# Performance work log

Hardware: AMD Instinct MI355X
Metric: run time of the kernel (lower is better)

## Reference

```python
import jax, jax.numpy as jnp
import numpy as np

BATCH = 16384
IN = 1024
OUT = 1024
SIGMA_MIN = 0.1
SIGMA_MAX = 1.0


def setup_inputs() -> dict:
    key = jax.random.key(0)
    k0, k1, k2, k3 = jax.random.split(key, 4)
    x = jax.random.normal(k0, (BATCH, IN), dtype=jnp.float32)
    # torch init: triu(randn) -> upper-triangular reflector banks
    U = jnp.triu(jax.random.normal(k1, (IN, IN), dtype=jnp.float32))
    V = jnp.triu(jax.random.normal(k2, (OUT, OUT), dtype=jnp.float32))
    p = 0.001 * jax.random.normal(k3, (min(IN, OUT),), dtype=jnp.float32)
    bias = jnp.zeros((OUT,), dtype=jnp.float32)
    return {"x": x, "U": U, "V": V, "p": p, "bias": bias}


def _hprod_step(x, u):
    # u has zeros in its first i entries (triu row i), so the full-vector
    # form equals torch's sliced Hprod on the last k = n - i columns.
    alpha = 2.0 * (x @ u) / jnp.dot(u, u)          # [bs]
    return x - alpha[:, None] * u[None, :], None   # rank-1 update


def reference(x, U, V, p, bias):
    r = (SIGMA_MAX - SIGMA_MIN) / 2.0
    sigma_mean = SIGMA_MIN + r
    # mask enforces torch slice semantics (entries below diag never used)
    Um = U * jnp.triu(jnp.ones_like(U))
    Vm = V * jnp.triu(jnp.ones_like(V))
    # Umultiply: reflectors i = 0 .. n_U-1 in order (sequential recurrence)
    x, _ = jax.lax.scan(_hprod_step, x, Um)
    # Sigma: diagonal scaling (square case IN == OUT)
    sigmas = 2.0 * r * (jax.nn.sigmoid(p) - 0.5) + sigma_mean
    x = x * sigmas[None, :]
    # Vmultiply: reflectors i = n_V-1 .. 0 (reverse order)
    x, _ = jax.lax.scan(_hprod_step, x, Vm[::-1])
    return x + bias
```

## Files before the change

kernel.cpp:

```cpp
#include <hip/hip_runtime.h>
#include <stdint.h>

typedef __attribute__((ext_vector_type(8))) short short8;
typedef __attribute__((ext_vector_type(4))) float f32x4;

#define NN 1024
#define NBATCH 16384
#define ME ((size_t)NN * NN)

__device__ __forceinline__ unsigned short f32_to_bf16_rne(float f) {
  unsigned int u = __float_as_uint(f);
  unsigned int r = (u + 0x7fffu + ((u >> 16) & 1u)) >> 16;
  return (unsigned short)r;
}

__device__ __forceinline__ unsigned int pack2bf(float lo, float hi) {
  return (unsigned int)f32_to_bf16_rne(lo) | ((unsigned int)f32_to_bf16_rne(hi) << 16);
}

__device__ __forceinline__ void split_bf16(float x, unsigned short& h, unsigned short& l) {
  h = f32_to_bf16_rne(x);
  float hf = __uint_as_float((unsigned int)h << 16);
  l = f32_to_bf16_rne(x - hf);
}

__device__ __forceinline__ float allsum64(float x) {
  x += __int_as_float(__builtin_amdgcn_update_dpp(0, __float_as_int(x), 0xB1, 0xF, 0xF, true));
  x += __int_as_float(__builtin_amdgcn_update_dpp(0, __float_as_int(x), 0x4E, 0xF, 0xF, true));
  x += __int_as_float(__builtin_amdgcn_update_dpp(0, __float_as_int(x), 0x141, 0xF, 0xF, true));
  x += __int_as_float(__builtin_amdgcn_update_dpp(0, __float_as_int(x), 0x140, 0xF, 0xF, true));
#if __has_builtin(__builtin_amdgcn_permlane16_swap) && __has_builtin(__builtin_amdgcn_permlane32_swap)
  {
    auto r16 = __builtin_amdgcn_permlane16_swap(__float_as_uint(x), __float_as_uint(x), false, false);
    x = __uint_as_float(r16[0]) + __uint_as_float(r16[1]);
    auto r32 = __builtin_amdgcn_permlane32_swap(__float_as_uint(x), __float_as_uint(x), false, false);
    x = __uint_as_float(r32[0]) + __uint_as_float(r32[1]);
  }
#else
  x += __int_as_float(__builtin_amdgcn_ds_swizzle(__float_as_int(x), 0x401F));
  x += __shfl_xor(x, 32);
#endif
  return x;
}

__global__ __launch_bounds__(256) void prep_kernel(
    const float* __restrict__ U, const float* __restrict__ V,
    const float* __restrict__ p, float* __restrict__ tau_u,
    float* __restrict__ tau_v, float* __restrict__ sigmas) {
  int wave = threadIdx.x >> 6, lane = threadIdx.x & 63;
  int row = blockIdx.x * 4 + wave;
  if (row < 2048) {
    const float* u = (row < NN) ? (U + (size_t)row * NN) : (V + (size_t)(row - NN) * NN);
    float s = 0.f;
#pragma unroll
    for (int t = 0; t < 16; ++t) { float a = u[lane + (t << 6)]; s += a * a; }
    s = allsum64(s);
    if (lane == 0) {
      float tau = 2.0f / s;
      if (row < NN) tau_u[row] = tau;
      else tau_v[row - NN] = tau;
    }
  } else if (row < 2064) {
    int j = ((row - 2048) << 6) + lane;
    float pj = p[j];
    float sg = 1.0f / (1.0f + expf(-pj));
    sigmas[j] = 0.9f * (sg - 0.5f) + 0.55f;
  }
}

__global__ __launch_bounds__(64) void gram_t8_kernel(
    const float* __restrict__ U, const float* __restrict__ V,
    const float* __restrict__ tau_u, const float* __restrict__ tau_v,
    float* __restrict__ T8all) {
  __shared__ float G[64];
  const int blk = blockIdx.x;
  const int lane = threadIdx.x;
  const float* bank;
  int rbase, rsign, st;
  if (blk < 128) { bank = U; rbase = 8 * blk; rsign = 1; st = 8 * blk; }
  else { int s = blk - 128; bank = V; rbase = 1023 - 8 * s; rsign = -1; st = 1016 - 8 * s; }

  if (lane < 28) {
    int j = 1, k = 0, t = lane;
    for (int jj = 1; jj < 8; ++jj) {
      int lo = jj * (jj - 1) / 2, hi = jj * (jj + 1) / 2;
      if (t >= lo && t < hi) { j = jj; k = t - lo; }
    }
    const float* rk = bank + (size_t)(rbase + rsign * k) * NN;
    const float* rj = bank + (size_t)(rbase + rsign * j) * NN;
    float acc = 0.f;
    for (int i = st >> 2; i < 256; ++i) {
      float4 a = *reinterpret_cast<const float4*>(rk + 4 * i);
      float4 b = *reinterpret_cast<const float4*>(rj + 4 * i);
      acc += a.x * b.x + a.y * b.y + a.z * b.z + a.w * b.w;
    }
    G[k * 8 + j] = acc;
  }
  __syncthreads();

  if (lane < 8) {
    float Tr[8];
#pragma unroll
    for (int j = 0; j < 8; ++j) Tr[j] = 0.f;
#pragma unroll
    for (int j = 0; j < 8; ++j) {
      int grow = rbase + rsign * j;
      float tj = (blk < 128) ? tau_u[grow] : tau_v[grow];
      float a = 0.f;
#pragma unroll
      for (int k = 0; k < 8; ++k) {
        if (k < j) a += Tr[k] * G[k * 8 + j];
      }
      Tr[j] = (lane == j) ? tj : (-tj * a);
    }
#pragma unroll
    for (int j = 0; j < 8; ++j) T8all[(size_t)blk * 64 + lane * 8 + j] = Tr[j];
  }
}

__global__ __launch_bounds__(256) void splity_kernel(
    const float* __restrict__ U, const float* __restrict__ V,
    unsigned short* __restrict__ Yhi, unsigned short* __restrict__ Ylo,
    unsigned short* __restrict__ YThi, unsigned short* __restrict__ YTlo) {
  __shared__ float ys[128][129];
  const int tid = threadIdx.x;
  const int c = blockIdx.x >> 3, et = blockIdx.x & 7;
  const int half = tid & 1;
  const int slot = tid >> 1;
  const int e0 = et << 7;
  const int grow = (c < 8) ? ((c << 7) + slot) : (1023 - ((c - 8) << 7) - slot);
  const float* src = ((c < 8) ? U : V) + (size_t)grow * NN + e0 + (half << 6);
#pragma unroll
  for (int i = 0; i < 16; ++i) {
    float4 v4 = *reinterpret_cast<const float4*>(src + (i << 2));
    const int kk = (half << 6) + (i << 2);
    ys[slot][kk + 0] = v4.x; ys[slot][kk + 1] = v4.y;
    ys[slot][kk + 2] = v4.z; ys[slot][kk + 3] = v4.w;
  }
  __syncthreads();
  {
    const size_t rbase = ((size_t)(c * 128 + slot)) * NN + e0 + (half << 6);
#pragma unroll
    for (int i = 0; i < 16; ++i) {
      const int kk = (half << 6) + (i << 2);
      ushort4 h4, l4;
      split_bf16(ys[slot][kk + 0], h4.x, l4.x);
      split_bf16(ys[slot][kk + 1], h4.y, l4.y);
      split_bf16(ys[slot][kk + 2], h4.z, l4.z);
      split_bf16(ys[slot][kk + 3], h4.w, l4.w);
      *reinterpret_cast<ushort4*>(&Yhi[rbase + (i << 2)]) = h4;
      *reinterpret_cast<ushort4*>(&Ylo[rbase + (i << 2)]) = l4;
    }
  }
  {
    const int e = slot;
    const size_t tbase = ((size_t)c * 1024 + e0 + e) * 128 + (half << 6);
#pragma unroll
    for (int i = 0; i < 16; ++i) {
      const int k0 = (half << 6) + (i << 2);
      ushort4 h4, l4;
      split_bf16(ys[k0 + 0][e], h4.x, l4.x);
      split_bf16(ys[k0 + 1][e], h4.y, l4.y);
      split_bf16(ys[k0 + 2][e], h4.z, l4.z);
      split_bf16(ys[k0 + 3][e], h4.w, l4.w);
      *reinterpret_cast<ushort4*>(&YThi[tbase + (i << 2)]) = h4;
      *reinterpret_cast<ushort4*>(&YTlo[tbase + (i << 2)]) = l4;
    }
  }
}

#define LDK 40

__global__ __launch_bounds__(256) void gramt_kernel(
    const unsigned short* __restrict__ Yhi, const unsigned short* __restrict__ Ylo,
    float* __restrict__ G) {
  __shared__ unsigned short Hs[128 * LDK];
  __shared__ unsigned short Ls[128 * LDK];
  const int tid = threadIdx.x;
  const int lane = tid & 63, wave = tid >> 6;
  const int c = blockIdx.x;
  const int wm = wave & 1, wn = wave >> 1;
  const int srow = tid >> 1, scol = (tid & 1) << 4;
  const unsigned short* ph = Yhi + ((size_t)(c * 128 + srow)) * NN + scol;
  const unsigned short* pl = Ylo + ((size_t)(c * 128 + srow)) * NN + scol;

  f32x4 acc[4][4];
#pragma unroll
  for (int a = 0; a < 4; ++a)
#pragma unroll
    for (int b = 0; b < 4; ++b) acc[a][b] = 0.f;

  const int arow0 = wm * 64, brow0 = wn * 64;
  const int fr = lane & 15, kb = (lane >> 4) << 3;

#pragma unroll 1
  for (int kt = 0; kt < 32; ++kt) {
    __syncthreads();
    *reinterpret_cast<uint4*>(&Hs[srow * LDK + scol]) = *reinterpret_cast<const uint4*>(ph + kt * 32);
    *reinterpret_cast<uint4*>(&Hs[srow * LDK + scol + 8]) = *reinterpret_cast<const uint4*>(ph + kt * 32 + 8);
    *reinterpret_cast<uint4*>(&Ls[srow * LDK + scol]) = *reinterpret_cast<const uint4*>(pl + kt * 32);
    *reinterpret_cast<uint4*>(&Ls[srow * LDK + scol + 8]) = *reinterpret_cast<const uint4*>(pl + kt * 32 + 8);
    __syncthreads();
    short8 ah[4], al[4], bh[4], bl[4];
#pragma unroll
    for (int tr = 0; tr < 4; ++tr) {
      ah[tr] = *reinterpret_cast<const short8*>(&Hs[(arow0 + tr * 16 + fr) * LDK + kb]);
      al[tr] = *reinterpret_cast<const short8*>(&Ls[(arow0 + tr * 16 + fr) * LDK + kb]);
    }
#pragma unroll
    for (int tc = 0; tc < 4; ++tc) {
      bh[tc] = *reinterpret_cast<const short8*>(&Hs[(brow0 + tc * 16 + fr) * LDK + kb]);
      bl[tc] = *reinterpret_cast<const short8*>(&Ls[(brow0 + tc * 16 + fr) * LDK + kb]);
    }
#pragma unroll
    for (int tr = 0; tr < 4; ++tr)
#pragma unroll
      for (int tc = 0; tc < 4; ++tc) {
        acc[tr][tc] = __builtin_amdgcn_mfma_f32_16x16x32_bf16(ah[tr], bh[tc], acc[tr][tc], 0, 0, 0);
        acc[tr][tc] = __builtin_amdgcn_mfma_f32_16x16x32_bf16(ah[tr], bl[tc], acc[tr][tc], 0, 0, 0);
        acc[tr][tc] = __builtin_amdgcn_mfma_f32_16x16x32_bf16(al[tr], bh[tc], acc[tr][tc], 0, 0, 0);
      }
  }
  const int rq = (lane >> 4) << 2;
#pragma unroll
  for (int tc = 0; tc < 4; ++tc) {
    const int gc = brow0 + tc * 16 + fr;
#pragma unroll
    for (int tr = 0; tr < 4; ++tr) {
      const int gr = arow0 + tr * 16 + rq;
#pragma unroll
      for (int q = 0; q < 4; ++q)
        G[((size_t)c * 128 + gr + q) * 128 + gc] = acc[tr][tc][q];
    }
  }
}

__global__ __launch_bounds__(256) void ttree_kernel(
    const float* __restrict__ G, const float* __restrict__ T8all,
    unsigned short* __restrict__ Thi, unsigned short* __restrict__ Tlo) {
  __shared__ float Ts[128 * 128];
  __shared__ float Gb[64 * 64];
  __shared__ float Xb[64 * 64];
  const int c = blockIdx.x, tid = threadIdx.x;
  for (int i = tid; i < 128 * 128; i += 256) Ts[i] = 0.f;
  __syncthreads();
  for (int i = tid; i < 1024; i += 256) {
    const int sb = i >> 6, ij = i & 63, r = ij >> 3, col = ij & 7;
    const int t8i = (c < 8) ? (16 * c + sb) : (128 + 16 * (c - 8) + sb);
    Ts[(8 * sb + r) * 128 + 8 * sb + col] = T8all[(size_t)t8i * 64 + ij];
  }
  __syncthreads();
  for (int b = 8; b <= 64; b <<= 1) {
    const int nm = 128 / (2 * b);
    for (int m = 0; m < nm; ++m) {
      const int a0 = 2 * b * m;
      for (int i = tid; i < b * b; i += 256) {
        const int r = i / b, cl = i % b;
        Gb[i] = G[((size_t)c * 128 + a0 + r) * 128 + a0 + b + cl];
      }
      __syncthreads();
      for (int i = tid; i < b * b; i += 256) {
        const int r = i / b, cl = i % b;
        float s = 0.f;
        for (int k = 0; k <= cl; ++k)
          s += Gb[r * b + k] * Ts[(a0 + b + k) * 128 + a0 + b + cl];
        Xb[i] = s;
      }
      __syncthreads();
      for (int i = tid; i < b * b; i += 256) {
        const int r = i / b, cl = i % b;
        float s = 0.f;
        for (int k = r; k < b; ++k)
          s -= Ts[(a0 + r) * 128 + a0 + k] * Xb[k * b + cl];
        Ts[(a0 + r) * 128 + a0 + b + cl] = s;
      }
      __syncthreads();
    }
  }
  for (int i = tid; i < 128 * 128; i += 256) {
    unsigned short h, l;
    split_bf16(Ts[i], h, l);
    Thi[(size_t)c * 128 * 128 + i] = h;
    Tlo[(size_t)c * 128 * 128 + i] = l;
  }
}

__global__ __launch_bounds__(256) void zw_kernel(
    const unsigned short* __restrict__ Thi, const unsigned short* __restrict__ Tlo,
    const unsigned short* __restrict__ YThi, const unsigned short* __restrict__ YTlo,
    unsigned short* __restrict__ WThi, unsigned short* __restrict__ WTlo) {
  __shared__ unsigned short Xh[128 * LDK], Xl[128 * LDK];
  __shared__ unsigned short Wh[128 * LDK], Wl[128 * LDK];
  const int tid = threadIdx.x;
  const int lane = tid & 63, wave = tid >> 6;
  const int c = blockIdx.x >> 3, bn = blockIdx.x & 7;
  const int n0 = bn * 128;
  const int wm = wave & 1, wn = wave >> 1;
  const int srow = tid >> 1, scol = (tid & 1) << 4;
  const unsigned short* pxh = Thi + ((size_t)c * 128 + srow) * 128 + scol;
  const unsigned short* pxl = Tlo + ((size_t)c * 128 + srow) * 128 + scol;
  const unsigned short* pwh = YThi + ((size_t)c * 1024 + n0 + srow) * 128 + scol;
  const unsigned short* pwl = YTlo + ((size_t)c * 1024 + n0 + srow) * 128 + scol;

  f32x4 acc[4][4];
#pragma unroll
  for (int a = 0; a < 4; ++a)
#pragma unroll
    for (int b = 0; b < 4; ++b) acc[a][b] = 0.f;

  const int arow0 = wm * 64, brow0 = wn * 64;
  const int fr = lane & 15, kb = (lane >> 4) << 3;

#pragma unroll 1
  for (int kt = 0; kt < 4; ++kt) {
    __syncthreads();
    *reinterpret_cast<uint4*>(&Xh[srow * LDK + scol]) = *reinterpret_cast<const uint4*>(pxh + kt * 32);
    *reinterpret_cast<uint4*>(&Xh[srow * LDK + scol + 8]) = *reinterpret_cast<const uint4*>(pxh + kt * 32 + 8);
    *reinterpret_cast<uint4*>(&Xl[srow * LDK + scol]) = *reinterpret_cast<const uint4*>(pxl + kt * 32);
    *reinterpret_cast<uint4*>(&Xl[srow * LDK + scol + 8]) = *reinterpret_cast<const uint4*>(pxl + kt * 32 + 8);
    *reinterpret_cast<uint4*>(&Wh[srow * LDK + scol]) = *reinterpret_cast<const uint4*>(pwh + kt * 32);
    *reinterpret_cast<uint4*>(&Wh[srow * LDK + scol + 8]) = *reinterpret_cast<const uint4*>(pwh + kt * 32 + 8);
    *reinterpret_cast<uint4*>(&Wl[srow * LDK + scol]) = *reinterpret_cast<const uint4*>(pwl + kt * 32);
    *reinterpret_cast<uint4*>(&Wl[srow * LDK + scol + 8]) = *reinterpret_cast<const uint4*>(pwl + kt * 32 + 8);
    __syncthreads();
    short8 ah[4], al[4], bh[4], bl[4];
#pragma unroll
    for (int tr = 0; tr < 4; ++tr) {
      ah[tr] = *reinterpret_cast<const short8*>(&Xh[(arow0 + tr * 16 + fr) * LDK + kb]);
      al[tr] = *reinterpret_cast<const short8*>(&Xl[(arow0 + tr * 16 + fr) * LDK + kb]);
    }
#pragma unroll
    for (int tc = 0; tc < 4; ++tc) {
      bh[tc] = *reinterpret_cast<const short8*>(&Wh[(brow0 + tc * 16 + fr) * LDK + kb]);
      bl[tc] = *reinterpret_cast<const short8*>(&Wl[(brow0 + tc * 16 + fr) * LDK + kb]);
    }
#pragma unroll
    for (int tr = 0; tr < 4; ++tr)
#pragma unroll
      for (int tc = 0; tc < 4; ++tc) {
        acc[tr][tc] = __builtin_amdgcn_mfma_f32_16x16x32_bf16(ah[tr], bh[tc], acc[tr][tc], 0, 0, 0);
        acc[tr][tc] = __builtin_amdgcn_mfma_f32_16x16x32_bf16(ah[tr], bl[tc], acc[tr][tc], 0, 0, 0);
        acc[tr][tc] = __builtin_amdgcn_mfma_f32_16x16x32_bf16(al[tr], bh[tc], acc[tr][tc], 0, 0, 0);
      }
  }
  const int rq = (lane >> 4) << 2;
#pragma unroll
  for (int tc = 0; tc < 4; ++tc) {
    const int gc = brow0 + tc * 16 + fr;
#pragma unroll
    for (int tr = 0; tr < 4; ++tr) {
      const int gr = arow0 + tr * 16 + rq;
      ushort4 h4, l4;
      split_bf16(acc[tr][tc][0], h4.x, l4.x);
      split_bf16(acc[tr][tc][1], h4.y, l4.y);
      split_bf16(acc[tr][tc][2], h4.z, l4.z);
      split_bf16(acc[tr][tc][3], h4.w, l4.w);
      const size_t off = ((size_t)c * 1024 + n0 + gc) * 128 + gr;
      *reinterpret_cast<ushort4*>(&WThi[off]) = h4;
      *reinterpret_cast<ushort4*>(&WTlo[off]) = l4;
    }
  }
}

__global__ __launch_bounds__(256) void chainc_kernel(
    const unsigned short* __restrict__ YThi, const unsigned short* __restrict__ YTlo,
    const unsigned short* __restrict__ WThi, const unsigned short* __restrict__ WTlo,
    unsigned short* __restrict__ chains) {
  __shared__ unsigned short Xh[128 * LDK], Xl[128 * LDK];
  __shared__ unsigned short Wh[128 * LDK], Wl[128 * LDK];
  const int tid = threadIdx.x;
  const int lane = tid & 63, wave = tid >> 6;
  const int c = blockIdx.x >> 6, b6 = blockIdx.x & 63;
  const int bm = b6 & 7, bn = b6 >> 3;
  const int m0 = bm * 128, n0 = bn * 128;
  const int wm = wave & 1, wn = wave >> 1;
  const int srow = tid >> 1, scol = (tid & 1) << 4;
  const unsigned short* pxh = YThi + ((size_t)c * 1024 + m0 + srow) * 128 + scol;
  const unsigned short* pxl = YTlo + ((size_t)c * 1024 + m0 + srow) * 128 + scol;
  const unsigned short* pwh = WThi + ((size_t)c * 1024 + n0 + srow) * 128 + scol;
  const unsigned short* pwl = WTlo + ((size_t)c * 1024 + n0 + srow) * 128 + scol;

  f32x4 acc[4][4];
#pragma unroll
  for (int a = 0; a < 4; ++a)
#pragma unroll
    for (int b = 0; b < 4; ++b) acc[a][b] = 0.f;

  const int arow0 = wm * 64, brow0 = wn * 64;
  const int fr = lane & 15, kb = (lane >> 4) << 3;

#pragma unroll 1
  for (int kt = 0; kt < 4; ++kt) {
    __syncthreads();
    *reinterpret_cast<uint4*>(&Xh[srow * LDK + scol]) = *reinterpret_cast<const uint4*>(pxh + kt * 32);
    *reinterpret_cast<uint4*>(&Xh[srow * LDK + scol + 8]) = *reinterpret_cast<const uint4*>(pxh + kt * 32 + 8);
    *reinterpret_cast<uint4*>(&Xl[srow * LDK + scol]) = *reinterpret_cast<const uint4*>(pxl + kt * 32);
    *reinterpret_cast<uint4*>(&Xl[srow * LDK + scol + 8]) = *reinterpret_cast<const uint4*>(pxl + kt * 32 + 8);
    *reinterpret_cast<uint4*>(&Wh[srow * LDK + scol]) = *reinterpret_cast<const uint4*>(pwh + kt * 32);
    *reinterpret_cast<uint4*>(&Wh[srow * LDK + scol + 8]) = *reinterpret_cast<const uint4*>(pwh + kt * 32 + 8);
    *reinterpret_cast<uint4*>(&Wl[srow * LDK + scol]) = *reinterpret_cast<const uint4*>(pwl + kt * 32);
    *reinterpret_cast<uint4*>(&Wl[srow * LDK + scol + 8]) = *reinterpret_cast<const uint4*>(pwl + kt * 32 + 8);
    __syncthreads();
    short8 ah[4], al[4], bh[4], bl[4];
#pragma unroll
    for (int tr = 0; tr < 4; ++tr) {
      ah[tr] = *reinterpret_cast<const short8*>(&Xh[(arow0 + tr * 16 + fr) * LDK + kb]);
      al[tr] = *reinterpret_cast<const short8*>(&Xl[(arow0 + tr * 16 + fr) * LDK + kb]);
    }
#pragma unroll
    for (int tc = 0; tc < 4; ++tc) {
      bh[tc] = *reinterpret_cast<const short8*>(&Wh[(brow0 + tc * 16 + fr) * LDK + kb]);
      bl[tc] = *reinterpret_cast<const short8*>(&Wl[(brow0 + tc * 16 + fr) * LDK + kb]);
    }
#pragma unroll
    for (int tr = 0; tr < 4; ++tr)
#pragma unroll
      for (int tc = 0; tc < 4; ++tc) {
        acc[tr][tc] = __builtin_amdgcn_mfma_f32_16x16x32_bf16(ah[tr], bh[tc], acc[tr][tc], 0, 0, 0);
        acc[tr][tc] = __builtin_amdgcn_mfma_f32_16x16x32_bf16(ah[tr], bl[tc], acc[tr][tc], 0, 0, 0);
        acc[tr][tc] = __builtin_amdgcn_mfma_f32_16x16x32_bf16(al[tr], bh[tc], acc[tr][tc], 0, 0, 0);
      }
  }
  unsigned short* dst = chains + (size_t)c * ME;
  const int rq = (lane >> 4) << 2;
  if ((c & 1) == 0) {
#pragma unroll
    for (int tc = 0; tc < 4; ++tc) {
      const int gcg = n0 + brow0 + tc * 16 + fr;
#pragma unroll
      for (int tr = 0; tr < 4; ++tr) {
        const int grg = m0 + arow0 + tr * 16 + rq;
#pragma unroll
        for (int q = 0; q < 4; ++q) {
          const float val = ((grg + q) == gcg ? 1.0f : 0.0f) - acc[tr][tc][q];
          dst[(size_t)(grg + q) * NN + gcg] = f32_to_bf16_rne(val);
        }
      }
    }
  } else {
#pragma unroll
    for (int tc = 0; tc < 4; ++tc) {
      const int gcg = n0 + brow0 + tc * 16 + fr;
#pragma unroll
      for (int tr = 0; tr < 4; ++tr) {
        const int grg = m0 + arow0 + tr * 16 + rq;
        ushort4 pk;
        pk.x = f32_to_bf16_rne(((grg + 0) == gcg ? 1.0f : 0.0f) - acc[tr][tc][0]);
        pk.y = f32_to_bf16_rne(((grg + 1) == gcg ? 1.0f : 0.0f) - acc[tr][tc][1]);
        pk.z = f32_to_bf16_rne(((grg + 2) == gcg ? 1.0f : 0.0f) - acc[tr][tc][2]);
        pk.w = f32_to_bf16_rne(((grg + 3) == gcg ? 1.0f : 0.0f) - acc[tr][tc][3]);
        *reinterpret_cast<ushort4*>(&dst[(size_t)gcg * NN + grg]) = pk;
      }
    }
  }
}

#define BM 128
#define BN 128
#define BK 32

__device__ __forceinline__ void compose_body(
    const unsigned short* __restrict__ Xb, const unsigned short* __restrict__ Wb,
    unsigned short* __restrict__ Op, const float* __restrict__ sig, int b, bool tstore) {
  __shared__ unsigned short As[BM * LDK];
  __shared__ unsigned short Bs[BN * LDK];
  const int tid = threadIdx.x;
  const int lane = tid & 63, wave = tid >> 6;
  const int bm = b & 7, bn = b >> 3;
  const int m0 = bm * BM, n0 = bn * BN;
  const int wm = wave & 1, wn = wave >> 1;

  const int srow = tid >> 1;
  const int scol = (tid & 1) << 4;
  const unsigned short* aptr = Xb + (size_t)(m0 + srow) * NN + scol;
  const unsigned short* bptr = Wb + (size_t)(n0 + srow) * NN + scol;

  f32x4 acc[4][4];
#pragma unroll
  for (int a = 0; a < 4; ++a)
#pragma unroll
    for (int bb = 0; bb < 4; ++bb) acc[a][bb] = 0.f;

  uint4 ra0 = *reinterpret_cast<const uint4*>(aptr + 0);
  uint4 ra1 = *reinterpret_cast<const uint4*>(aptr + 8);
  uint4 rb0 = *reinterpret_cast<const uint4*>(bptr + 0);
  uint4 rb1 = *reinterpret_cast<const uint4*>(bptr + 8);

  const int arow0 = wm * 64;
  const int brow0 = wn * 64;
  const int fr = lane & 15;
  const int kb = (lane >> 4) << 3;

#pragma unroll 1
  for (int kt = 0; kt < NN / BK; ++kt) {
    __syncthreads();
    *reinterpret_cast<uint4*>(&As[srow * LDK + scol]) = ra0;
    *reinterpret_cast<uint4*>(&As[srow * LDK + scol + 8]) = ra1;
    *reinterpret_cast<uint4*>(&Bs[srow * LDK + scol]) = rb0;
    *reinterpret_cast<uint4*>(&Bs[srow * LDK + scol + 8]) = rb1;
    __syncthreads();
    if (kt + 1 < NN / BK) {
      const unsigned short* ap = aptr + (kt + 1) * BK;
      const unsigned short* bp = bptr + (kt + 1) * BK;
      ra0 = *reinterpret_cast<const uint4*>(ap + 0);
      ra1 = *reinterpret_cast<const uint4*>(ap + 8);
      rb0 = *reinterpret_cast<const uint4*>(bp + 0);
      rb1 = *reinterpret_cast<const uint4*>(bp + 8);
    }
    short8 af[4], bf[4];
#pragma unroll
    for (int tr = 0; tr < 4; ++tr)
      af[tr] = *reinterpret_cast<const short8*>(&As[(arow0 + tr * 16 + fr) * LDK + kb]);
#pragma unroll
    for (int tc = 0; tc < 4; ++tc)
      bf[tc] = *reinterpret_cast<const short8*>(&Bs[(brow0 + tc * 16 + fr) * LDK + kb]);
#pragma unroll
    for (int tr = 0; tr < 4; ++tr)
#pragma unroll
      for (int tc = 0; tc < 4; ++tc)
        acc[tr][tc] = __builtin_amdgcn_mfma_f32_16x16x32_bf16(af[tr], bf[tc], acc[tr][tc], 0, 0, 0);
  }

  const int rq = (lane >> 4) << 2;
  if (!tstore) {
#pragma unroll
    for (int tc = 0; tc < 4; ++tc) {
      const int gc = n0 + brow0 + tc * 16 + fr;
      const float s = sig ? sig[gc] : 1.0f;
#pragma unroll
      for (int tr = 0; tr < 4; ++tr) {
        const int gr = m0 + arow0 + tr * 16 + rq;
#pragma unroll
        for (int q = 0; q < 4; ++q) {
          Op[(size_t)(gr + q) * NN + gc] = f32_to_bf16_rne(acc[tr][tc][q] * s);
        }
      }
    }
  } else {
#pragma unroll
    for (int tc = 0; tc < 4; ++tc) {
      const int gc = n0 + brow0 + tc * 16 + fr;
#pragma unroll
      for (int tr = 0; tr < 4; ++tr) {
        const int gr = m0 + arow0 + tr * 16 + rq;
        ushort4 pk;
        pk.x = f32_to_bf16_rne(acc[tr][tc][0]);
        pk.y = f32_to_bf16_rne(acc[tr][tc][1]);
        pk.z = f32_to_bf16_rne(acc[tr][tc][2]);
        pk.w = f32_to_bf16_rne(acc[tr][tc][3]);
        *reinterpret_cast<ushort4*>(&Op[(size_t)gc * NN + gr]) = pk;
      }
    }
  }
}

__global__ __launch_bounds__(256) void composeL1_kernel(
    const unsigned short* __restrict__ ch, unsigned short* __restrict__ P) {
  const int sub = blockIdx.x >> 6, b = blockIdx.x & 63;
  const int i = sub & 3;
  const unsigned short* x = ch + (size_t)((sub < 4 ? 0 : 8) + 2 * i) * ME;
  compose_body(x, x + ME, P + (size_t)sub * ME, nullptr, b, (i & 1) != 0);
}

__global__ __launch_bounds__(256) void composeL2_kernel(
    const unsigned short* __restrict__ P, unsigned short* __restrict__ Q) {
  const int sub = blockIdx.x >> 6, b = blockIdx.x & 63;
  compose_body(P + (size_t)(2 * sub) * ME, P + (size_t)(2 * sub + 1) * ME,
               Q + (size_t)sub * ME, nullptr, b, (sub & 1) != 0);
}

__global__ __launch_bounds__(256) void composeL3_kernel(
    const unsigned short* __restrict__ Q, const float* __restrict__ sigmas,
    unsigned short* __restrict__ F) {
  const int sub = blockIdx.x >> 6, b = blockIdx.x & 63;
  if (sub == 0) compose_body(Q, Q + ME, F, sigmas, b, false);
  else compose_body(Q + 2 * ME, Q + 3 * ME, F + ME, nullptr, b, true);
}

__global__ __launch_bounds__(256) void composeL4_kernel(
    const unsigned short* __restrict__ F, unsigned short* __restrict__ Mt) {
  compose_body(F + ME, F, Mt, nullptr, blockIdx.x, false);
}

__global__ __launch_bounds__(256) void gemm_kernel(
    const float* __restrict__ X, const unsigned short* __restrict__ Mt,
    const float* __restrict__ bias, float* __restrict__ Out) {
  __shared__ unsigned short As[BM * LDK];
  __shared__ unsigned short Bs[BN * LDK];
  const int tid = threadIdx.x;
  const int lane = tid & 63, wave = tid >> 6;
  const int bm = blockIdx.x & 127;
  const int bn = blockIdx.x >> 7;
  const int m0 = bm * BM, n0 = bn * BN;
  const int wm = wave & 1, wn = wave >> 1;

  const int srow = tid >> 1;
  const int scol = (tid & 1) << 4;
  const float* aptr = X + (size_t)(m0 + srow) * NN + scol;
  const unsigned short* bptr = Mt + (size_t)(n0 + srow) * NN + scol;

  f32x4 acc[4][4];
#pragma unroll
  for (int a = 0; a < 4; ++a)
#pragma unroll
    for (int b = 0; b < 4; ++b) acc[a][b] = 0.f;

  float4 ra0 = *reinterpret_cast<const float4*>(aptr + 0);
  float4 ra1 = *reinterpret_cast<const float4*>(aptr + 4);
  float4 ra2 = *reinterpret_cast<const float4*>(aptr + 8);
  float4 ra3 = *reinterpret_cast<const float4*>(aptr + 12);
  uint4 rb0 = *reinterpret_cast<const uint4*>(bptr + 0);
  uint4 rb1 = *reinterpret_cast<const uint4*>(bptr + 8);

  const int arow0 = wm * 64;
  const int brow0 = wn * 64;
  const int fr = lane & 15;
  const int kb = (lane >> 4) << 3;

#pragma unroll 1
  for (int kt = 0; kt < NN / BK; ++kt) {
    __syncthreads();
    uint4 w0, w1;
    w0.x = pack2bf(ra0.x, ra0.y); w0.y = pack2bf(ra0.z, ra0.w);
    w0.z = pack2bf(ra1.x, ra1.y); w0.w = pack2bf(ra1.z, ra1.w);
    w1.x = pack2bf(ra2.x, ra2.y); w1.y = pack2bf(ra2.z, ra2.w);
    w1.z = pack2bf(ra3.x, ra3.y); w1.w = pack2bf(ra3.z, ra3.w);
    *reinterpret_cast<uint4*>(&As[srow * LDK + scol]) = w0;
    *reinterpret_cast<uint4*>(&As[srow * LDK + scol + 8]) = w1;
    *reinterpret_cast<uint4*>(&Bs[srow * LDK + scol]) = rb0;
    *reinterpret_cast<uint4*>(&Bs[srow * LDK + scol + 8]) = rb1;
    __syncthreads();
    if (kt + 1 < NN / BK) {
      const float* ap = aptr + (kt + 1) * BK;
      const unsigned short* bp = bptr + (kt + 1) * BK;
      ra0 = *reinterpret_cast<const float4*>(ap + 0);
      ra1 = *reinterpret_cast<const float4*>(ap + 4);
      ra2 = *reinterpret_cast<const float4*>(ap + 8);
      ra3 = *reinterpret_cast<const float4*>(ap + 12);
      rb0 = *reinterpret_cast<const uint4*>(bp + 0);
      rb1 = *reinterpret_cast<const uint4*>(bp + 8);
    }
    short8 af[4], bf[4];
#pragma unroll
    for (int tr = 0; tr < 4; ++tr)
      af[tr] = *reinterpret_cast<const short8*>(&As[(arow0 + tr * 16 + fr) * LDK + kb]);
#pragma unroll
    for (int tc = 0; tc < 4; ++tc)
      bf[tc] = *reinterpret_cast<const short8*>(&Bs[(brow0 + tc * 16 + fr) * LDK + kb]);
#pragma unroll
    for (int tr = 0; tr < 4; ++tr)
#pragma unroll
      for (int tc = 0; tc < 4; ++tc)
        acc[tr][tc] = __builtin_amdgcn_mfma_f32_16x16x32_bf16(af[tr], bf[tc], acc[tr][tc], 0, 0, 0);
  }

  const int rq = (lane >> 4) << 2;
#pragma unroll
  for (int tc = 0; tc < 4; ++tc) {
    const int gc = n0 + brow0 + tc * 16 + fr;
    const float bv = bias[gc];
#pragma unroll
    for (int tr = 0; tr < 4; ++tr) {
      const int gr = m0 + arow0 + tr * 16 + rq;
#pragma unroll
      for (int q = 0; q < 4; ++q) {
        Out[(size_t)(gr + q) * NN + gc] = acc[tr][tc][q] + bv;
      }
    }
  }
}

extern "C" void kernel_launch(void* const* d_in, const int* in_sizes, int n_in,
                              void* d_out, int out_size, void* d_ws, size_t ws_size,
                              hipStream_t stream) {
  const float* x = (const float*)d_in[0];
  const float* U = (const float*)d_in[1];
  const float* V = (const float*)d_in[2];
  const float* p = (const float*)d_in[3];
  const float* bias = (const float*)d_in[4];
  float* out = (float*)d_out;

  char* ws = (char*)d_ws;
  float* tau_u = (float*)(ws);
  float* tau_v = (float*)(ws + 4096);
  float* sigmas = (float*)(ws + 8192);
  float* T8all = (float*)(ws + 16384);
  unsigned short* Mt = (unsigned short*)(ws + 81920);

  unsigned short* sc = (unsigned short*)d_out;
  unsigned short* chains = sc;
  unsigned short* P = sc + 16 * ME;
  unsigned short* Q = sc + 24 * ME;
  unsigned short* F = sc + 28 * ME;
  unsigned short* YThi = sc + 16 * ME;
  unsigned short* YTlo = sc + 18 * ME;
  unsigned short* WThi = sc + 20 * ME;
  unsigned short* WTlo = sc + 22 * ME;
  unsigned short* Yhi = sc + 24 * ME;
  unsigned short* Ylo = sc + 26 * ME;
  float* G = (float*)(sc + 28 * ME);
  unsigned short* Thi = sc + 28 * ME + 524288;
  unsigned short* Tlo = Thi + 262144;

  prep_kernel<<<516, 256, 0, stream>>>(U, V, p, tau_u, tau_v, sigmas);
  gram_t8_kernel<<<256, 64, 0, stream>>>(U, V, tau_u, tau_v, T8all);
  splity_kernel<<<128, 256, 0, stream>>>(U, V, Yhi, Ylo, YThi, YTlo);
  gramt_kernel<<<16, 256, 0, stream>>>(Yhi, Ylo, G);
  ttree_kernel<<<16, 256, 0, stream>>>(G, T8all, Thi, Tlo);
  zw_kernel<<<128, 256, 0, stream>>>(Thi, Tlo, YThi, YTlo, WThi, WTlo);
  chainc_kernel<<<1024, 256, 0, stream>>>(YThi, YTlo, WThi, WTlo, chains);
  composeL1_kernel<<<512, 256, 0, stream>>>(chains, P);
  composeL2_kernel<<<256, 256, 0, stream>>>(P, Q);
  composeL3_kernel<<<128, 256, 0, stream>>>(Q, sigmas, F);
  composeL4_kernel<<<64, 256, 0, stream>>>(F, Mt);
  gemm_kernel<<<1024, 256, 0, stream>>>(x, Mt, bias, out);
}
```

Before: 360.4 us.

## Split-K the gram kernel and double-buffer LDS in compose and GEMM loops

The gram kernel is split along K into 8 slices, so 128 blocks run instead of 16. It writes partial Gram matrices, and ttree sums them when it loads each block, with the T buffers moved to a different scratch region to make room. The compose and final GEMM main loops now use two LDS buffers and issue one barrier per K-step instead of two, so the global prefetch two steps ahead overlaps the MFMA work. In exchange this doubles LDS use per block, which may lower occupancy, and adds the traffic for the partial-sum buffers.

```diff
diff --git a/kernel.cpp b/kernel.cpp
--- a/kernel.cpp
+++ b/kernel.cpp
@@ -170,19 +170,39 @@
 }
 
 #define LDK 40
+#define BM 128
+#define BN 128
+#define BK 32
+
+__device__ __forceinline__ void tile_compute(
+    const unsigned short* __restrict__ As, const unsigned short* __restrict__ Bs,
+    f32x4 acc[4][4], int arow0, int brow0, int fr, int kb) {
+  short8 af[4], bf[4];
+#pragma unroll
+  for (int tr = 0; tr < 4; ++tr)
+    af[tr] = *reinterpret_cast<const short8*>(&As[(arow0 + tr * 16 + fr) * LDK + kb]);
+#pragma unroll
+  for (int tc = 0; tc < 4; ++tc)
+    bf[tc] = *reinterpret_cast<const short8*>(&Bs[(brow0 + tc * 16 + fr) * LDK + kb]);
+#pragma unroll
+  for (int tr = 0; tr < 4; ++tr)
+#pragma unroll
+    for (int tc = 0; tc < 4; ++tc)
+      acc[tr][tc] = __builtin_amdgcn_mfma_f32_16x16x32_bf16(af[tr], bf[tc], acc[tr][tc], 0, 0, 0);
+}
 
 __global__ __launch_bounds__(256) void gramt_kernel(
     const unsigned short* __restrict__ Yhi, const unsigned short* __restrict__ Ylo,
-    float* __restrict__ G) {
+    float* __restrict__ Gp) {
   __shared__ unsigned short Hs[128 * LDK];
   __shared__ unsigned short Ls[128 * LDK];
   const int tid = threadIdx.x;
   const int lane = tid & 63, wave = tid >> 6;
-  const int c = blockIdx.x;
+  const int c = blockIdx.x >> 3, ks = blockIdx.x & 7;
   const int wm = wave & 1, wn = wave >> 1;
   const int srow = tid >> 1, scol = (tid & 1) << 4;
-  const unsigned short* ph = Yhi + ((size_t)(c * 128 + srow)) * NN + scol;
-  const unsigned short* pl = Ylo + ((size_t)(c * 128 + srow)) * NN + scol;
+  const unsigned short* ph = Yhi + ((size_t)(c * 128 + srow)) * NN + ks * 128 + scol;
+  const unsigned short* pl = Ylo + ((size_t)(c * 128 + srow)) * NN + ks * 128 + scol;
 
   f32x4 acc[4][4];
 #pragma unroll
@@ -194,7 +214,7 @@
   const int fr = lane & 15, kb = (lane >> 4) << 3;
 
 #pragma unroll 1
-  for (int kt = 0; kt < 32; ++kt) {
+  for (int kt = 0; kt < 4; ++kt) {
     __syncthreads();
     *reinterpret_cast<uint4*>(&Hs[srow * LDK + scol]) = *reinterpret_cast<const uint4*>(ph + kt * 32);
     *reinterpret_cast<uint4*>(&Hs[srow * LDK + scol + 8]) = *reinterpret_cast<const uint4*>(ph + kt * 32 + 8);
@@ -230,13 +250,13 @@
       const int gr = arow0 + tr * 16 + rq;
 #pragma unroll
       for (int q = 0; q < 4; ++q)
-        G[((size_t)c * 128 + gr + q) * 128 + gc] = acc[tr][tc][q];
+        Gp[(((size_t)c * 8 + ks) * 128 + gr + q) * 128 + gc] = acc[tr][tc][q];
     }
   }
 }
 
 __global__ __launch_bounds__(256) void ttree_kernel(
-    const float* __restrict__ G, const float* __restrict__ T8all,
+    const float* __restrict__ Gp, const float* __restrict__ T8all,
     unsigned short* __restrict__ Thi, unsigned short* __restrict__ Tlo) {
   __shared__ float Ts[128 * 128];
   __shared__ float Gb[64 * 64];
@@ -256,7 +276,11 @@
       const int a0 = 2 * b * m;
       for (int i = tid; i < b * b; i += 256) {
         const int r = i / b, cl = i % b;
-        Gb[i] = G[((size_t)c * 128 + a0 + r) * 128 + a0 + b + cl];
+        float s = 0.f;
+#pragma unroll
+        for (int sl = 0; sl < 8; ++sl)
+          s += Gp[(((size_t)c * 8 + sl) * 128 + a0 + r) * 128 + a0 + b + cl];
+        Gb[i] = s;
       }
       __syncthreads();
       for (int i = tid; i < b * b; i += 256) {
@@ -455,15 +479,11 @@
   }
 }
 
-#define BM 128
-#define BN 128
-#define BK 32
-
 __device__ __forceinline__ void compose_body(
     const unsigned short* __restrict__ Xb, const unsigned short* __restrict__ Wb,
     unsigned short* __restrict__ Op, const float* __restrict__ sig, int b, bool tstore) {
-  __shared__ unsigned short As[BM * LDK];
-  __shared__ unsigned short Bs[BN * LDK];
+  __shared__ unsigned short As[2][BM * LDK];
+  __shared__ unsigned short Bs[2][BN * LDK];
   const int tid = threadIdx.x;
   const int lane = tid & 63, wave = tid >> 6;
   const int bm = b & 7, bn = b >> 3;
@@ -481,45 +501,44 @@
 #pragma unroll
     for (int bb = 0; bb < 4; ++bb) acc[a][bb] = 0.f;
 
-  uint4 ra0 = *reinterpret_cast<const uint4*>(aptr + 0);
-  uint4 ra1 = *reinterpret_cast<const uint4*>(aptr + 8);
-  uint4 rb0 = *reinterpret_cast<const uint4*>(bptr + 0);
-  uint4 rb1 = *reinterpret_cast<const uint4*>(bptr + 8);
+  uint4 raE0 = *reinterpret_cast<const uint4*>(aptr + 0);
+  uint4 raE1 = *reinterpret_cast<const uint4*>(aptr + 8);
+  uint4 rbE0 = *reinterpret_cast<const uint4*>(bptr + 0);
+  uint4 rbE1 = *reinterpret_cast<const uint4*>(bptr + 8);
+  uint4 raO0 = *reinterpret_cast<const uint4*>(aptr + BK);
+  uint4 raO1 = *reinterpret_cast<const uint4*>(aptr + BK + 8);
+  uint4 rbO0 = *reinterpret_cast<const uint4*>(bptr + BK);
+  uint4 rbO1 = *reinterpret_cast<const uint4*>(bptr + BK + 8);
 
   const int arow0 = wm * 64;
   const int brow0 = wn * 64;
   const int fr = lane & 15;
   const int kb = (lane >> 4) << 3;
 
+#define CB_STEP(PB, RA0, RA1, RB0, RB1, KT)                                    \
+  {                                                                            \
+    *reinterpret_cast<uint4*>(&As[PB][srow * LDK + scol]) = RA0;               \
+    *reinterpret_cast<uint4*>(&As[PB][srow * LDK + scol + 8]) = RA1;           \
+    *reinterpret_cast<uint4*>(&Bs[PB][srow * LDK + scol]) = RB0;               \
+    *reinterpret_cast<uint4*>(&Bs[PB][srow * LDK + scol + 8]) = RB1;           \
+    if ((KT) + 2 < 32) {                                                       \
+      RA0 = *reinterpret_cast<const uint4*>(aptr + ((KT) + 2) * BK);           \
+      RA1 = *reinterpret_cast<const uint4*>(aptr + ((KT) + 2) * BK + 8);       \
+      RB0 = *reinterpret_cast<const uint4*>(bptr + ((KT) + 2) * BK);           \
+      RB1 = *reinterpret_cast<const uint4*>(bptr + ((KT) + 2) * BK + 8);       \
+    }                                                                          \
+    asm volatile("s_waitcnt lgkmcnt(0)" ::: "memory");                         \
+    __builtin_amdgcn_s_barrier();                                              \
+    __builtin_amdgcn_sched_barrier(0);                                         \
+    tile_compute(&As[PB][0], &Bs[PB][0], acc, arow0, brow0, fr, kb);           \
+  }
+
 #pragma unroll 1
-  for (int kt = 0; kt < NN / BK; ++kt) {
-    __syncthreads();
-    *reinterpret_cast<uint4*>(&As[srow * LDK + scol]) = ra0;
-    *reinterpret_cast<uint4*>(&As[srow * LDK + scol + 8]) = ra1;
-    *reinterpret_cast<uint4*>(&Bs[srow * LDK + scol]) = rb0;
-    *reinterpret_cast<uint4*>(&Bs[srow * LDK + scol + 8]) = rb1;
-    __syncthreads();
-    if (kt + 1 < NN / BK) {
-      const unsigned short* ap = aptr + (kt + 1) * BK;
-      const unsigned short* bp = bptr + (kt + 1) * BK;
-      ra0 = *reinterpret_cast<const uint4*>(ap + 0);
-      ra1 = *reinterpret_cast<const uint4*>(ap + 8);
-      rb0 = *reinterpret_cast<const uint4*>(bp + 0);
-      rb1 = *reinterpret_cast<const uint4*>(bp + 8);
-    }
-    short8 af[4], bf[4];
-#pragma unroll
-    for (int tr = 0; tr < 4; ++tr)
-      af[tr] = *reinterpret_cast<const short8*>(&As[(arow0 + tr * 16 + fr) * LDK + kb]);
-#pragma unroll
-    for (int tc = 0; tc < 4; ++tc)
-      bf[tc] = *reinterpret_cast<const short8*>(&Bs[(brow0 + tc * 16 + fr) * LDK + kb]);
-#pragma unroll
-    for (int tr = 0; tr < 4; ++tr)
-#pragma unroll
-      for (int tc = 0; tc < 4; ++tc)
-        acc[tr][tc] = __builtin_amdgcn_mfma_f32_16x16x32_bf16(af[tr], bf[tc], acc[tr][tc], 0, 0, 0);
-  }
+  for (int kt2 = 0; kt2 < 16; ++kt2) {
+    CB_STEP(0, raE0, raE1, rbE0, rbE1, 2 * kt2)
+    CB_STEP(1, raO0, raO1, rbO0, rbO1, 2 * kt2 + 1)
+  }
+#undef CB_STEP
 
   const int rq = (lane >> 4) << 2;
   if (!tstore) {
@@ -585,8 +604,8 @@
 __global__ __launch_bounds__(256) void gemm_kernel(
     const float* __restrict__ X, const unsigned short* __restrict__ Mt,
     const float* __restrict__ bias, float* __restrict__ Out) {
-  __shared__ unsigned short As[BM * LDK];
-  __shared__ unsigned short Bs[BN * LDK];
+  __shared__ unsigned short As[2][BM * LDK];
+  __shared__ unsigned short Bs[2][BN * LDK];
   const int tid = threadIdx.x;
   const int lane = tid & 63, wave = tid >> 6;
   const int bm = blockIdx.x & 127;
@@ -605,54 +624,57 @@
 #pragma unroll
     for (int b = 0; b < 4; ++b) acc[a][b] = 0.f;
 
-  float4 ra0 = *reinterpret_cast<const float4*>(aptr + 0);
-  float4 ra1 = *reinterpret_cast<const float4*>(aptr + 4);
-  float4 ra2 = *reinterpret_cast<const float4*>(aptr + 8);
-  float4 ra3 = *reinterpret_cast<const float4*>(aptr + 12);
-  uint4 rb0 = *reinterpret_cast<const uint4*>(bptr + 0);
-  uint4 rb1 = *reinterpret_cast<const uint4*>(bptr + 8);
+  float4 rE0 = *reinterpret_cast<const float4*>(aptr + 0);
+  float4 rE1 = *reinterpret_cast<const float4*>(aptr + 4);
+  float4 rE2 = *reinterpret_cast<const float4*>(aptr + 8);
+  float4 rE3 = *reinterpret_cast<const float4*>(aptr + 12);
+  uint4 bE0 = *reinterpret_cast<const uint4*>(bptr + 0);
+  uint4 bE1 = *reinterpret_cast<const uint4*>(bptr + 8);
+  float4 rO0 = *reinterpret_cast<const float4*>(aptr + BK);
+  float4 rO1 = *reinterpret_cast<const float4*>(aptr + BK + 4);
+  float4 rO2 = *reinterpret_cast<const float4*>(aptr + BK + 8);
+  float4 rO3 = *reinterpret_cast<const float4*>(aptr + BK + 12);
+  uint4 bO0 = *reinterpret_cast<const uint4*>(bptr + BK);
+  uint4 bO1 = *reinterpret_cast<const uint4*>(bptr + BK + 8);
 
   const int arow0 = wm * 64;
   const int brow0 = wn * 64;
   const int fr = lane & 15;
   const int kb = (lane >> 4) << 3;
 
+#define GM_STEP(PB, A0, A1, A2, A3, B0, B1, KT)                                \
+  {                                                                            \
+    uint4 w0, w1;                                                              \
+    w0.x = pack2bf(A0.x, A0.y); w0.y = pack2bf(A0.z, A0.w);                    \
+    w0.z = pack2bf(A1.x, A1.y); w0.w = pack2bf(A1.z, A1.w);                    \
+    w1.x = pack2bf(A2.x, A2.y); w1.y = pack2bf(A2.z, A2.w);                    \
+    w1.z = pack2bf(A3.x, A3.y); w1.w = pack2bf(A3.z, A3.w);                    \
+    *reinterpret_cast<uint4*>(&As[PB][srow * LDK + scol]) = w0;                \
+    *reinterpret_cast<uint4*>(&As[PB][srow * LDK + scol + 8]) = w1;            \
+    *reinterpret_cast<uint4*>(&Bs[PB][srow * LDK + scol]) = B0;                \
+    *reinterpret_cast<uint4*>(&Bs[PB][srow * LDK + scol + 8]) = B1;            \
+    if ((KT) + 2 < 32) {                                                       \
+      const float* ap = aptr + ((KT) + 2) * BK;                                \
+      const unsigned short* bp = bptr + ((KT) + 2) * BK;                       \
+      A0 = *reinterpret_cast<const float4*>(ap + 0);                           \
+      A1 = *reinterpret_cast<const float4*>(ap + 4);                           \
+      A2 = *reinterpret_cast<const float4*>(ap + 8);                           \
+      A3 = *reinterpret_cast<const float4*>(ap + 12);                          \
+      B0 = *reinterpret_cast<const uint4*>(bp + 0);                            \
+      B1 = *reinterpret_cast<const uint4*>(bp + 8);                            \
+    }                                                                          \
+    asm volatile("s_waitcnt lgkmcnt(0)" ::: "memory");                         \
+    __builtin_amdgcn_s_barrier();                                              \
+    __builtin_amdgcn_sched_barrier(0);                                         \
+    tile_compute(&As[PB][0], &Bs[PB][0], acc, arow0, brow0, fr, kb);           \
+  }
+
 #pragma unroll 1
-  for (int kt = 0; kt < NN / BK; ++kt) {
-    __syncthreads();
-    uint4 w0, w1;
-    w0.x = pack2bf(ra0.x, ra0.y); w0.y = pack2bf(ra0.z, ra0.w);
-    w0.z = pack2bf(ra1.x, ra1.y); w0.w = pack2bf(ra1.z, ra1.w);
-    w1.x = pack2bf(ra2.x, ra2.y); w1.y = pack2bf(ra2.z, ra2.w);
-    w1.z = pack2bf(ra3.x, ra3.y); w1.w = pack2bf(ra3.z, ra3.w);
-    *reinterpret_cast<uint4*>(&As[srow * LDK + scol]) = w0;
-    *reinterpret_cast<uint4*>(&As[srow * LDK + scol + 8]) = w1;
-    *reinterpret_cast<uint4*>(&Bs[srow * LDK + scol]) = rb0;
-    *reinterpret_cast<uint4*>(&Bs[srow * LDK + scol + 8]) = rb1;
-    __syncthreads();
-    if (kt + 1 < NN / BK) {
-      const float* ap = aptr + (kt + 1) * BK;
-      const unsigned short* bp = bptr + (kt + 1) * BK;
-      ra0 = *reinterpret_cast<const float4*>(ap + 0);
-      ra1 = *reinterpret_cast<const float4*>(ap + 4);
-      ra2 = *reinterpret_cast<const float4*>(ap + 8);
-      ra3 = *reinterpret_cast<const float4*>(ap + 12);
-      rb0 = *reinterpret_cast<const uint4*>(bp + 0);
-      rb1 = *reinterpret_cast<const uint4*>(bp + 8);
-    }
-    short8 af[4], bf[4];
-#pragma unroll
-    for (int tr = 0; tr < 4; ++tr)
-      af[tr] = *reinterpret_cast<const short8*>(&As[(arow0 + tr * 16 + fr) * LDK + kb]);
-#pragma unroll
-    for (int tc = 0; tc < 4; ++tc)
-      bf[tc] = *reinterpret_cast<const short8*>(&Bs[(brow0 + tc * 16 + fr) * LDK + kb]);
-#pragma unroll
-    for (int tr = 0; tr < 4; ++tr)
-#pragma unroll
-      for (int tc = 0; tc < 4; ++tc)
-        acc[tr][tc] = __builtin_amdgcn_mfma_f32_16x16x32_bf16(af[tr], bf[tc], acc[tr][tc], 0, 0, 0);
-  }
+  for (int kt2 = 0; kt2 < 16; ++kt2) {
+    GM_STEP(0, rE0, rE1, rE2, rE3, bE0, bE1, 2 * kt2)
+    GM_STEP(1, rO0, rO1, rO2, rO3, bO0, bO1, 2 * kt2 + 1)
+  }
+#undef GM_STEP
 
   const int rq = (lane >> 4) << 2;
 #pragma unroll
@@ -698,15 +720,15 @@
   unsigned short* WTlo = sc + 22 * ME;
   unsigned short* Yhi = sc + 24 * ME;
   unsigned short* Ylo = sc + 26 * ME;
-  float* G = (float*)(sc + 28 * ME);
-  unsigned short* Thi = sc + 28 * ME + 524288;
+  float* Gp = (float*)(sc + 28 * ME);
+  unsigned short* Thi = sc + 24 * ME;
   unsigned short* Tlo = Thi + 262144;
 
   prep_kernel<<<516, 256, 0, stream>>>(U, V, p, tau_u, tau_v, sigmas);
   gram_t8_kernel<<<256, 64, 0, stream>>>(U, V, tau_u, tau_v, T8all);
   splity_kernel<<<128, 256, 0, stream>>>(U, V, Yhi, Ylo, YThi, YTlo);
-  gramt_kernel<<<16, 256, 0, stream>>>(Yhi, Ylo, G);
-  ttree_kernel<<<16, 256, 0, stream>>>(G, T8all, Thi, Tlo);
+  gramt_kernel<<<128, 256, 0, stream>>>(Yhi, Ylo, Gp);
+  ttree_kernel<<<16, 256, 0, stream>>>(Gp, T8all, Thi, Tlo);
   zw_kernel<<<128, 256, 0, stream>>>(Thi, Tlo, YThi, YTlo, WThi, WTlo);
   chainc_kernel<<<1024, 256, 0, stream>>>(YThi, YTlo, WThi, WTlo, chains);
   composeL1_kernel<<<512, 256, 0, stream>>>(chains, P);
```

Result: faster. 340.7 us (-5.5%).
